# Performance work log

Hardware: AMD Instinct MI355X
Metric: run time of the kernel (lower is better)

Reference implementation:

```python
import jax, jax.numpy as jnp
import numpy as np
from jax import lax

H = 32   # hidden_size
L = 8    # num_layers
D_IN = 64    # lstm input_size / fc0 out
FEAT = 4096  # feature_size
T = 300      # frame_size
B = 64       # batch


def setup_inputs() -> dict:
    key = jax.random.key(0)
    ks = jax.random.split(key, 16)
    s = 0.05
    inp = {
        "x": jax.random.normal(ks[0], (B, T, FEAT), dtype=jnp.float32),
        # fc0: Linear(4096->64), ReLU, Dropout(eval), Linear(64->64)
        "W0": jax.random.normal(ks[1], (D_IN, FEAT), dtype=jnp.float32) * s,
        "b0": jax.random.normal(ks[2], (D_IN,), dtype=jnp.float32) * s,
        "W1": jax.random.normal(ks[3], (D_IN, D_IN), dtype=jnp.float32) * s,
        "b1": jax.random.normal(ks[4], (D_IN,), dtype=jnp.float32) * s,
        # LSTM params, PyTorch layout: W_ih [4H, in], W_hh [4H, H], biases [4H]
        "Wih0": jax.random.normal(ks[5], (4 * H, D_IN), dtype=jnp.float32) * s,
        "Wih": jax.random.normal(ks[6], (L - 1, 4 * H, H), dtype=jnp.float32) * s,
        "Whh": jax.random.normal(ks[7], (L, 4 * H, H), dtype=jnp.float32) * s,
        "bih": jax.random.normal(ks[8], (L, 4 * H), dtype=jnp.float32) * s,
        "bhh": jax.random.normal(ks[9], (L, 4 * H), dtype=jnp.float32) * s,
        # fc1: 32 -> 1 ; fc2: 300 -> 1
        "Wfc1": jax.random.normal(ks[10], (1, H), dtype=jnp.float32) * s,
        "bfc1": jax.random.normal(ks[11], (1,), dtype=jnp.float32) * s,
        "Wfc2": jax.random.normal(ks[12], (1, T), dtype=jnp.float32) * s,
        "bfc2": jax.random.normal(ks[13], (1,), dtype=jnp.float32) * s,
    }
    return inp


def _lstm_layer(x_seq, Wih_l, Whh_l, bih_l, bhh_l):
    # x_seq: [B, T, in] -> h_seq: [B, T, H]; PyTorch gate order i,f,g,o
    gx = jnp.einsum('bti,gi->btg', x_seq, Wih_l) + bih_l  # [B,T,4H]
    b = x_seq.shape[0]
    init = (jnp.zeros((b, H), x_seq.dtype), jnp.zeros((b, H), x_seq.dtype))

    def step(carry, gx_t):
        h, c = carry
        g = gx_t + h @ Whh_l.T + bhh_l
        i, f, gg, o = jnp.split(g, 4, axis=-1)
        c = jax.nn.sigmoid(f) * c + jax.nn.sigmoid(i) * jnp.tanh(gg)
        h = jax.nn.sigmoid(o) * jnp.tanh(c)
        return (h, c), h

    _, hs = lax.scan(step, init, jnp.swapaxes(gx, 0, 1))  # hs: [T,B,H]
    return jnp.swapaxes(hs, 0, 1)


def reference(x, W0, b0, W1, b1, Wih0, Wih, Whh, bih, bhh, Wfc1, bfc1, Wfc2, bfc2):
    # fc0 (dropout is identity in eval mode)
    h = jax.nn.relu(jnp.einsum('btf,of->bto', x, W0) + b0)
    h = jnp.einsum('bti,oi->bto', h, W1) + b1  # [B,T,64]
    # stacked LSTM, h0=c0=0
    for l in range(L):
        Wih_l = Wih0 if l == 0 else Wih[l - 1]
        h = _lstm_layer(h, Wih_l, Whh[l], bih[l], bhh[l])  # [B,T,32]
    # fc1 over hidden, squeeze, fc2 over time, squeeze
    y = jnp.einsum('bth,oh->bto', h, Wfc1)[..., 0] + bfc1[0]  # [B,T]
    y = y @ Wfc2.T + bfc2  # [B,1]
    return y[:, 0]
```

## Files before the change

### kernel.cpp

```cpp
#include <hip/hip_runtime.h>
#include <cstdint>

#define FEAT 4096
#define DIN  64
#define HS   32
#define NL   8
#define TT   300
#define BB   64
#define G4   128
#define MROWS (BB*TT)
#define KS    4
#define KSLICE (FEAT/KS)
#define BK    64
#define NCHUNK (KSLICE/BK)

typedef __bf16 bf16x8 __attribute__((ext_vector_type(8)));
typedef float  f32x4  __attribute__((ext_vector_type(4)));
typedef unsigned short u16x8 __attribute__((ext_vector_type(8)));

__device__ __forceinline__ float sigm(float x){ return __fdividef(1.f, 1.f + __expf(-x)); }
__device__ __forceinline__ float tanh_f(float x){ return __fdividef(2.f, 1.f + __expf(-2.f*x)) - 1.f; }

__device__ __forceinline__ unsigned short bf16_rne(float f){
    uint32_t u = __float_as_uint(f);
    return (unsigned short)((u + 0x7FFFu + ((u >> 16) & 1u)) >> 16);
}

__global__ __launch_bounds__(256) void w0split(const float* __restrict__ W0,
                                               unsigned short* __restrict__ wh,
                                               unsigned short* __restrict__ wl)
{
    const int i = (blockIdx.x * 256 + threadIdx.x) * 4;
    float4 v = *(const float4*)(W0 + i);
    float f[4] = {v.x, v.y, v.z, v.w};
    unsigned short hh[4], ll[4];
    #pragma unroll
    for (int j = 0; j < 4; ++j) {
        unsigned short h = bf16_rne(f[j]);
        float fh = __uint_as_float((uint32_t)h << 16);
        hh[j] = h;
        ll[j] = bf16_rne(f[j] - fh);
    }
    *(ushort4*)(wh + i) = make_ushort4(hh[0], hh[1], hh[2], hh[3]);
    *(ushort4*)(wl + i) = make_ushort4(ll[0], ll[1], ll[2], ll[3]);
}

__global__ __launch_bounds__(256, 2) void fc_gemm1(
    const float* __restrict__ x,
    const unsigned short* __restrict__ wh,
    const unsigned short* __restrict__ wl,
    float* __restrict__ part)
{
    __shared__ __align__(16) unsigned short xh[2][64][64];
    __shared__ __align__(16) unsigned short xl[2][64][64];
    __shared__ __align__(16) unsigned short wh_s[2][64][64];
    __shared__ __align__(16) unsigned short wl_s[2][64][64];

    const int t   = threadIdx.x;
    const int l   = t & 63;
    const int w   = t >> 6;
    const int rbb = (w >> 1) * 32;
    const int cbb = (w & 1) * 32;
    const int r0  = blockIdx.x * 64;
    const int kb0 = blockIdx.y * KSLICE;

    const int srow = t >> 3;
    const int sg   = t & 7;

    f32x4 acc[2][2];
    #pragma unroll
    for (int i = 0; i < 2; ++i)
        #pragma unroll
        for (int j = 0; j < 2; ++j)
            acc[i][j] = (f32x4){0.f, 0.f, 0.f, 0.f};

    float4 xr[2][2];
    uint4  w0h[2], w0l[2];

    auto LOAD = [&](int c) {
        const float* xb = x + (size_t)r0 * FEAT + kb0 + c * BK;
        xr[0][0] = *(const float4*)(xb + (size_t)srow * FEAT + sg * 8);
        xr[0][1] = *(const float4*)(xb + (size_t)srow * FEAT + sg * 8 + 4);
        xr[1][0] = *(const float4*)(xb + (size_t)(srow + 32) * FEAT + sg * 8);
        xr[1][1] = *(const float4*)(xb + (size_t)(srow + 32) * FEAT + sg * 8 + 4);
        const int wo = kb0 + c * BK + sg * 8;
        w0h[0] = *(const uint4*)(wh + (size_t)srow * FEAT + wo);
        w0h[1] = *(const uint4*)(wh + (size_t)(srow + 32) * FEAT + wo);
        w0l[0] = *(const uint4*)(wl + (size_t)srow * FEAT + wo);
        w0l[1] = *(const uint4*)(wl + (size_t)(srow + 32) * FEAT + wo);
    };

    auto STORE = [&](int c) {
        const int buf = c & 1;
        #pragma unroll
        for (int j = 0; j < 2; ++j) {
            const int row = srow + j * 32;
            const int gsw = (sg ^ (row & 7)) * 8;
            float f0[8] = {xr[j][0].x, xr[j][0].y, xr[j][0].z, xr[j][0].w,
                           xr[j][1].x, xr[j][1].y, xr[j][1].z, xr[j][1].w};
            u16x8 vh, vl;
            #pragma unroll
            for (int i = 0; i < 8; ++i) {
                uint32_t u  = __float_as_uint(f0[i]);
                uint32_t rh = (u + 0x7FFFu + ((u >> 16) & 1u)) >> 16;
                vh[i] = (unsigned short)rh;
                float fl = f0[i] - __uint_as_float(rh << 16);
                uint32_t u2 = __float_as_uint(fl);
                vl[i] = (unsigned short)((u2 + 0x7FFFu + ((u2 >> 16) & 1u)) >> 16);
            }
            *(u16x8*)&xh[buf][row][gsw] = vh;
            *(u16x8*)&xl[buf][row][gsw] = vl;
            *(uint4*)&wh_s[buf][row][gsw] = w0h[j];
            *(uint4*)&wl_s[buf][row][gsw] = w0l[j];
        }
    };

    auto COMPUTE = [&](int buf) {
        #pragma unroll
        for (int kstep = 0; kstep < 2; ++kstep) {
            const int gA = kstep * 4 + (l >> 4);
            bf16x8 Ah[2], Al[2], Bh[2], Bl[2];
            #pragma unroll
            for (int rf = 0; rf < 2; ++rf) {
                const int ra  = rbb + rf * 16 + (l & 15);
                const int off = (gA ^ (ra & 7)) * 8;
                Ah[rf] = __builtin_bit_cast(bf16x8, *(const u16x8*)&xh[buf][ra][off]);
                Al[rf] = __builtin_bit_cast(bf16x8, *(const u16x8*)&xl[buf][ra][off]);
            }
            #pragma unroll
            for (int cf = 0; cf < 2; ++cf) {
                const int cb  = cbb + cf * 16 + (l & 15);
                const int off = (gA ^ (cb & 7)) * 8;
                Bh[cf] = __builtin_bit_cast(bf16x8, *(const u16x8*)&wh_s[buf][cb][off]);
                Bl[cf] = __builtin_bit_cast(bf16x8, *(const u16x8*)&wl_s[buf][cb][off]);
            }
            #pragma unroll
            for (int rf = 0; rf < 2; ++rf)
                #pragma unroll
                for (int cf = 0; cf < 2; ++cf) {
                    acc[rf][cf] = __builtin_amdgcn_mfma_f32_16x16x32_bf16(Ah[rf], Bh[cf], acc[rf][cf], 0, 0, 0);
                    acc[rf][cf] = __builtin_amdgcn_mfma_f32_16x16x32_bf16(Al[rf], Bh[cf], acc[rf][cf], 0, 0, 0);
                    acc[rf][cf] = __builtin_amdgcn_mfma_f32_16x16x32_bf16(Ah[rf], Bl[cf], acc[rf][cf], 0, 0, 0);
                }
        }
    };

    LOAD(0);
    for (int c = 0; c < NCHUNK; ++c) {
        STORE(c);
        if (c + 1 < NCHUNK) LOAD(c + 1);
        asm volatile("s_waitcnt lgkmcnt(0)" ::: "memory");
        __builtin_amdgcn_s_barrier();
        COMPUTE(c & 1);
    }

    #pragma unroll
    for (int rf = 0; rf < 2; ++rf)
        #pragma unroll
        for (int cf = 0; cf < 2; ++cf)
            #pragma unroll
            for (int r = 0; r < 4; ++r) {
                const int row = r0 + rbb + rf * 16 + (l >> 4) * 4 + r;
                const int col = cbb + cf * 16 + (l & 15);
                part[((size_t)blockIdx.y * MROWS + row) * 64 + col] = acc[rf][cf][r];
            }
}

__global__ __launch_bounds__(256) void fc_tail(
    const float* __restrict__ part, const float* __restrict__ b0,
    const float* __restrict__ W1, const float* __restrict__ b1,
    const float* __restrict__ Wih0,
    const float* __restrict__ bih, const float* __restrict__ bhh,
    float* __restrict__ gx0)
{
    __shared__ __align__(16) float h1s[64][68];
    __shared__ __align__(16) float h2s[64][68];

    const int tid = threadIdx.x;
    const int tc  = tid & 15;
    const int tr  = tid >> 4;
    const int r0  = blockIdx.x * 64;

    {
        const int row = tid >> 2;
        const int c0  = (tid & 3) * 16;
        float4 s[4];
        #pragma unroll
        for (int i = 0; i < 4; ++i)
            s[i] = *(const float4*)(part + ((size_t)(r0 + row)) * 64 + c0 + 4 * i);
        #pragma unroll
        for (int ks = 1; ks < KS; ++ks)
            #pragma unroll
            for (int i = 0; i < 4; ++i) {
                float4 v = *(const float4*)(part + ((size_t)ks * MROWS + r0 + row) * 64 + c0 + 4 * i);
                s[i].x += v.x; s[i].y += v.y; s[i].z += v.z; s[i].w += v.w;
            }
        #pragma unroll
        for (int i = 0; i < 4; ++i) {
            float4 bv = *(const float4*)(b0 + c0 + 4 * i);
            float4 o;
            o.x = fmaxf(s[i].x + bv.x, 0.f);
            o.y = fmaxf(s[i].y + bv.y, 0.f);
            o.z = fmaxf(s[i].z + bv.z, 0.f);
            o.w = fmaxf(s[i].w + bv.w, 0.f);
            *(float4*)&h1s[row][c0 + 4 * i] = o;
        }
    }
    __syncthreads();

    float acc2[4][4] = {};
    #pragma unroll
    for (int k4 = 0; k4 < 16; ++k4) {
        const int k = k4 * 4;
        float4 a[4], wv[4];
        #pragma unroll
        for (int i = 0; i < 4; ++i) a[i] = *(const float4*)&h1s[tr * 4 + i][k];
        #pragma unroll
        for (int j = 0; j < 4; ++j) wv[j] = *(const float4*)(W1 + (size_t)(tc * 4 + j) * DIN + k);
        #pragma unroll
        for (int i = 0; i < 4; ++i)
            #pragma unroll
            for (int j = 0; j < 4; ++j)
                acc2[i][j] += a[i].x * wv[j].x + a[i].y * wv[j].y + a[i].z * wv[j].z + a[i].w * wv[j].w;
    }
    __syncthreads();
    #pragma unroll
    for (int i = 0; i < 4; ++i)
        #pragma unroll
        for (int j = 0; j < 4; ++j)
            h2s[tr * 4 + i][tc * 4 + j] = acc2[i][j] + b1[tc * 4 + j];
    __syncthreads();

    #pragma unroll
    for (int p = 0; p < 2; ++p) {
        float acc3[4][4] = {};
        #pragma unroll
        for (int k4 = 0; k4 < 16; ++k4) {
            const int k = k4 * 4;
            float4 a[4], wv[4];
            #pragma unroll
            for (int i = 0; i < 4; ++i) a[i] = *(const float4*)&h2s[tr * 4 + i][k];
            #pragma unroll
            for (int j = 0; j < 4; ++j) wv[j] = *(const float4*)(Wih0 + (size_t)(p * 64 + tc * 4 + j) * DIN + k);
            #pragma unroll
            for (int i = 0; i < 4; ++i)
                #pragma unroll
                for (int j = 0; j < 4; ++j)
                    acc3[i][j] += a[i].x * wv[j].x + a[i].y * wv[j].y + a[i].z * wv[j].z + a[i].w * wv[j].w;
        }
        const int g0 = p * 64 + tc * 4;
        #pragma unroll
        for (int i = 0; i < 4; ++i) {
            float4 ov;
            ov.x = acc3[i][0] + bih[g0 + 0] + bhh[g0 + 0];
            ov.y = acc3[i][1] + bih[g0 + 1] + bhh[g0 + 1];
            ov.z = acc3[i][2] + bih[g0 + 2] + bhh[g0 + 2];
            ov.w = acc3[i][3] + bih[g0 + 3] + bhh[g0 + 3];
            *(float4*)(gx0 + (size_t)(r0 + tr * 4 + i) * G4 + g0) = ov;
        }
    }
}

__global__ __launch_bounds__(512, 2) void lstm_all(
    const float* __restrict__ gx0,
    const float* __restrict__ Wih, const float* __restrict__ Whh,
    const float* __restrict__ bih, const float* __restrict__ bhh,
    const float* __restrict__ Wfc1, const float* __restrict__ bfc1,
    const float* __restrict__ Wfc2, const float* __restrict__ bfc2,
    float* __restrict__ out)
{
    const int b    = blockIdx.x;
    const int tid  = threadIdx.x;
    const int l    = tid >> 6;
    const int lane = tid & 63;
    const int q0   = lane;
    const int q1   = lane + 64;

    __shared__ __align__(16) float hbuf[NL][2][HS];
    __shared__ __align__(16) float gbuf[NL][G4];
    __shared__ __align__(16) float h7[TT][HS];
    __shared__ float red[NL];

    float whh0[HS], whh1[HS], wih0[HS], wih1[HS];
    {
        const float* whhl = Whh + (size_t)l * G4 * HS;
        const float* wihl = Wih + (size_t)(l > 0 ? l - 1 : 0) * G4 * HS;
        #pragma unroll
        for (int k4 = 0; k4 < 8; ++k4) {
            float4 v0 = *(const float4*)(whhl + q0 * HS + 4 * k4);
            float4 v1 = *(const float4*)(whhl + q1 * HS + 4 * k4);
            whh0[4*k4+0]=v0.x; whh0[4*k4+1]=v0.y; whh0[4*k4+2]=v0.z; whh0[4*k4+3]=v0.w;
            whh1[4*k4+0]=v1.x; whh1[4*k4+1]=v1.y; whh1[4*k4+2]=v1.z; whh1[4*k4+3]=v1.w;
            float4 u0 = *(const float4*)(wihl + q0 * HS + 4 * k4);
            float4 u1 = *(const float4*)(wihl + q1 * HS + 4 * k4);
            wih0[4*k4+0]=u0.x; wih0[4*k4+1]=u0.y; wih0[4*k4+2]=u0.z; wih0[4*k4+3]=u0.w;
            wih1[4*k4+0]=u1.x; wih1[4*k4+1]=u1.y; wih1[4*k4+2]=u1.z; wih1[4*k4+3]=u1.w;
        }
    }
    const float bias0 = (l > 0) ? (bih[l*G4 + q0] + bhh[l*G4 + q0]) : 0.f;
    const float bias1 = (l > 0) ? (bih[l*G4 + q1] + bhh[l*G4 + q1]) : 0.f;

    float c_state = 0.f;

    const float* gxb = gx0 + (size_t)b * TT * G4;
    float pf0 = 0.f, pf1 = 0.f;
    if (l == 0) { pf0 = gxb[q0]; pf1 = gxb[q1]; }

    for (int s = 0; s < TT + NL - 1; ++s) {
        const int t = s - l;
        if (0 <= t && t < TT) {
            float acc0, acc1;
            if (l == 0) {
                acc0 = pf0; acc1 = pf1;
                const int tn = t + 1;
                if (tn < TT) { pf0 = gxb[(size_t)tn * G4 + q0]; pf1 = gxb[(size_t)tn * G4 + q1]; }
            } else {
                acc0 = bias0; acc1 = bias1;
            }
            float a0a = 0.f, a0b = 0.f, a1a = 0.f, a1b = 0.f;
            if (t > 0) {
                const float4* hp = (const float4*)hbuf[l][(t - 1) & 1];
                #pragma unroll
                for (int k4 = 0; k4 < 8; ++k4) {
                    float4 v = hp[k4];
                    a0a = fmaf(whh0[4*k4+0], v.x, a0a); a0b = fmaf(whh0[4*k4+1], v.y, a0b);
                    a0a = fmaf(whh0[4*k4+2], v.z, a0a); a0b = fmaf(whh0[4*k4+3], v.w, a0b);
                    a1a = fmaf(whh1[4*k4+0], v.x, a1a); a1b = fmaf(whh1[4*k4+1], v.y, a1b);
                    a1a = fmaf(whh1[4*k4+2], v.z, a1a); a1b = fmaf(whh1[4*k4+3], v.w, a1b);
                }
            }
            if (l > 0) {
                const float4* hq = (const float4*)hbuf[l - 1][t & 1];
                #pragma unroll
                for (int k4 = 0; k4 < 8; ++k4) {
                    float4 v = hq[k4];
                    a0a = fmaf(wih0[4*k4+0], v.x, a0a); a0b = fmaf(wih0[4*k4+1], v.y, a0b);
                    a0a = fmaf(wih0[4*k4+2], v.z, a0a); a0b = fmaf(wih0[4*k4+3], v.w, a0b);
                    a1a = fmaf(wih1[4*k4+0], v.x, a1a); a1b = fmaf(wih1[4*k4+1], v.y, a1b);
                    a1a = fmaf(wih1[4*k4+2], v.z, a1a); a1b = fmaf(wih1[4*k4+3], v.w, a1b);
                }
            }
            acc0 += a0a + a0b;
            acc1 += a1a + a1b;
            gbuf[l][q0] = acc0;
            gbuf[l][q1] = acc1;
            asm volatile("s_waitcnt lgkmcnt(0)" ::: "memory");
            if (lane < HS) {
                const float ig = gbuf[l][lane];
                const float fg = gbuf[l][HS + lane];
                const float gg = gbuf[l][2*HS + lane];
                const float og = gbuf[l][3*HS + lane];
                c_state = sigm(fg) * c_state + sigm(ig) * tanh_f(gg);
                const float hv = sigm(og) * tanh_f(c_state);
                hbuf[l][t & 1][lane] = hv;
                if (l == NL - 1) h7[t][lane] = hv;
            }
        }
        __syncthreads();
    }

    float part = 0.f;
    for (int t = tid; t < TT; t += 512) {
        float st = 0.f;
        #pragma unroll
        for (int j = 0; j < HS; ++j) st = fmaf(h7[t][j], Wfc1[j], st);
        part += (st + bfc1[0]) * Wfc2[t];
    }
    #pragma unroll
    for (int off = 32; off >= 1; off >>= 1) part += __shfl_down(part, off, 64);
    if (lane == 0) red[l] = part;
    __syncthreads();
    if (tid == 0) {
        float tot = 0.f;
        #pragma unroll
        for (int w = 0; w < NL; ++w) tot += red[w];
        out[b] = tot + bfc2[0];
    }
}

extern "C" void kernel_launch(void* const* d_in, const int* in_sizes, int n_in,
                              void* d_out, int out_size, void* d_ws, size_t ws_size,
                              hipStream_t stream) {
    const float* x    = (const float*)d_in[0];
    const float* W0   = (const float*)d_in[1];
    const float* b0   = (const float*)d_in[2];
    const float* W1   = (const float*)d_in[3];
    const float* b1   = (const float*)d_in[4];
    const float* Wih0 = (const float*)d_in[5];
    const float* Wih  = (const float*)d_in[6];
    const float* Whh  = (const float*)d_in[7];
    const float* bih  = (const float*)d_in[8];
    const float* bhh  = (const float*)d_in[9];
    const float* Wfc1 = (const float*)d_in[10];
    const float* bfc1 = (const float*)d_in[11];
    const float* Wfc2 = (const float*)d_in[12];
    const float* bfc2 = (const float*)d_in[13];

    char* wsb = (char*)d_ws;
    float*          gx0 = (float*)wsb;
    unsigned short* wh  = (unsigned short*)(wsb + 9830400);
    unsigned short* wl  = (unsigned short*)(wsb + 9830400 + 524288);
    float*          prt = (float*)(wsb + 9830400 + 1048576);

    w0split <<<256, 256, 0, stream>>>(W0, wh, wl);
    fc_gemm1<<<dim3(MROWS / 64, KS), 256, 0, stream>>>(x, wh, wl, prt);
    fc_tail <<<MROWS / 64, 256, 0, stream>>>(prt, b0, W1, b1, Wih0, bih, bhh, gx0);
    lstm_all<<<BB, 512, 0, stream>>>(gx0, Wih, Whh, bih, bhh, Wfc1, bfc1, Wfc2, bfc2,
                                     (float*)d_out);
}
```

Baseline: 432.3 us.

## Split LSTM gate dot products across half-waves and reduce with shuffles

Each lane now computes all four gates for one hidden unit over half of the K dimension, and the two halves are combined with a cross-half shuffle. This removes the shared-memory gate buffer round trip and the lgkmcnt wait inside every recurrent step. The fc_tail output is interleaved per hidden unit so layer 0 fetches its four gate inputs with one float4 load. Weight loads go through pinned inline-asm loads and launch bounds drop to one block per CU, which could raise register pressure or change scheduling.

```diff
diff --git a/kernel.cpp b/kernel.cpp
--- a/kernel.cpp
+++ b/kernel.cpp
@@ -26,6 +26,20 @@
     return (unsigned short)((u + 0x7FFFu + ((u >> 16) & 1u)) >> 16);
 }
 
+__device__ __forceinline__ void ld4_pin(const float* p0, const float* p1,
+                                        const float* p2, const float* p3,
+                                        float4& a, float4& b, float4& c, float4& d) {
+    asm volatile(
+        "global_load_dwordx4 %0, %4, off\n\t"
+        "global_load_dwordx4 %1, %5, off\n\t"
+        "global_load_dwordx4 %2, %6, off\n\t"
+        "global_load_dwordx4 %3, %7, off\n\t"
+        "s_waitcnt vmcnt(0)"
+        : "=&v"(a), "=&v"(b), "=&v"(c), "=&v"(d)
+        : "v"(p0), "v"(p1), "v"(p2), "v"(p3)
+        : "memory");
+}
+
 __global__ __launch_bounds__(256) void w0split(const float* __restrict__ W0,
                                                unsigned short* __restrict__ wh,
                                                unsigned short* __restrict__ wl)
@@ -171,7 +185,7 @@
     const float* __restrict__ W1, const float* __restrict__ b1,
     const float* __restrict__ Wih0,
     const float* __restrict__ bih, const float* __restrict__ bhh,
-    float* __restrict__ gx0)
+    float* __restrict__ gxp)
 {
     __shared__ __align__(16) float h1s[64][68];
     __shared__ __align__(16) float h2s[64][68];
@@ -251,18 +265,20 @@
         const int g0 = p * 64 + tc * 4;
         #pragma unroll
         for (int i = 0; i < 4; ++i) {
-            float4 ov;
-            ov.x = acc3[i][0] + bih[g0 + 0] + bhh[g0 + 0];
-            ov.y = acc3[i][1] + bih[g0 + 1] + bhh[g0 + 1];
-            ov.z = acc3[i][2] + bih[g0 + 2] + bhh[g0 + 2];
-            ov.w = acc3[i][3] + bih[g0 + 3] + bhh[g0 + 3];
-            *(float4*)(gx0 + (size_t)(r0 + tr * 4 + i) * G4 + g0) = ov;
-        }
-    }
-}
-
-__global__ __launch_bounds__(512, 2) void lstm_all(
-    const float* __restrict__ gx0,
+            #pragma unroll
+            for (int jj = 0; jj < 4; ++jj) {
+                const int cc  = tc * 4 + jj;
+                const int m   = cc & 31;
+                const int gi  = p * 2 + (cc >> 5);
+                const float v = acc3[i][jj] + bih[g0 + jj] + bhh[g0 + jj];
+                gxp[(size_t)(r0 + tr * 4 + i) * G4 + m * 4 + gi] = v;
+            }
+        }
+    }
+}
+
+__global__ __launch_bounds__(512, 1) void lstm_all(
+    const float* __restrict__ gxp,
     const float* __restrict__ Wih, const float* __restrict__ Whh,
     const float* __restrict__ bih, const float* __restrict__ bhh,
     const float* __restrict__ Wfc1, const float* __restrict__ bfc1,
@@ -273,85 +289,109 @@
     const int tid  = threadIdx.x;
     const int l    = tid >> 6;
     const int lane = tid & 63;
-    const int q0   = lane;
-    const int q1   = lane + 64;
+    const int m    = lane & 31;
+    const int k0   = (lane >> 5) * 16;
 
     __shared__ __align__(16) float hbuf[NL][2][HS];
-    __shared__ __align__(16) float gbuf[NL][G4];
     __shared__ __align__(16) float h7[TT][HS];
     __shared__ float red[NL];
 
-    float whh0[HS], whh1[HS], wih0[HS], wih1[HS];
+    float4 wh4[4][4], wi4[4][4];
     {
-        const float* whhl = Whh + (size_t)l * G4 * HS;
-        const float* wihl = Wih + (size_t)(l > 0 ? l - 1 : 0) * G4 * HS;
-        #pragma unroll
-        for (int k4 = 0; k4 < 8; ++k4) {
-            float4 v0 = *(const float4*)(whhl + q0 * HS + 4 * k4);
-            float4 v1 = *(const float4*)(whhl + q1 * HS + 4 * k4);
-            whh0[4*k4+0]=v0.x; whh0[4*k4+1]=v0.y; whh0[4*k4+2]=v0.z; whh0[4*k4+3]=v0.w;
-            whh1[4*k4+0]=v1.x; whh1[4*k4+1]=v1.y; whh1[4*k4+2]=v1.z; whh1[4*k4+3]=v1.w;
-            float4 u0 = *(const float4*)(wihl + q0 * HS + 4 * k4);
-            float4 u1 = *(const float4*)(wihl + q1 * HS + 4 * k4);
-            wih0[4*k4+0]=u0.x; wih0[4*k4+1]=u0.y; wih0[4*k4+2]=u0.z; wih0[4*k4+3]=u0.w;
-            wih1[4*k4+0]=u1.x; wih1[4*k4+1]=u1.y; wih1[4*k4+2]=u1.z; wih1[4*k4+3]=u1.w;
-        }
-    }
-    const float bias0 = (l > 0) ? (bih[l*G4 + q0] + bhh[l*G4 + q0]) : 0.f;
-    const float bias1 = (l > 0) ? (bih[l*G4 + q1] + bhh[l*G4 + q1]) : 0.f;
+        const float* wb = Whh + (size_t)l * G4 * HS;
+        #pragma unroll
+        for (int j = 0; j < 4; ++j) {
+            const float* rp = wb + (size_t)(j * 32 + m) * HS + k0;
+            ld4_pin(rp, rp + 4, rp + 8, rp + 12,
+                    wh4[j][0], wh4[j][1], wh4[j][2], wh4[j][3]);
+        }
+    }
+    if (l > 0) {
+        const float* wb = Wih + (size_t)(l - 1) * G4 * HS;
+        #pragma unroll
+        for (int j = 0; j < 4; ++j) {
+            const float* rp = wb + (size_t)(j * 32 + m) * HS + k0;
+            ld4_pin(rp, rp + 4, rp + 8, rp + 12,
+                    wi4[j][0], wi4[j][1], wi4[j][2], wi4[j][3]);
+        }
+    } else {
+        #pragma unroll
+        for (int j = 0; j < 4; ++j)
+            #pragma unroll
+            for (int q = 0; q < 4; ++q)
+                wi4[j][q] = make_float4(0.f, 0.f, 0.f, 0.f);
+    }
+
+    float bias[4] = {0.f, 0.f, 0.f, 0.f};
+    if (l > 0) {
+        #pragma unroll
+        for (int j = 0; j < 4; ++j)
+            bias[j] = bih[l * G4 + j * 32 + m] + bhh[l * G4 + j * 32 + m];
+    }
 
     float c_state = 0.f;
 
-    const float* gxb = gx0 + (size_t)b * TT * G4;
-    float pf0 = 0.f, pf1 = 0.f;
-    if (l == 0) { pf0 = gxb[q0]; pf1 = gxb[q1]; }
+    const float* gxb = gxp + (size_t)b * TT * G4;
+    float4 pf = make_float4(0.f, 0.f, 0.f, 0.f);
+    if (l == 0) pf = *(const float4*)(gxb + m * 4);
 
     for (int s = 0; s < TT + NL - 1; ++s) {
         const int t = s - l;
         if (0 <= t && t < TT) {
-            float acc0, acc1;
+            float4 gin;
             if (l == 0) {
-                acc0 = pf0; acc1 = pf1;
+                gin = pf;
                 const int tn = t + 1;
-                if (tn < TT) { pf0 = gxb[(size_t)tn * G4 + q0]; pf1 = gxb[(size_t)tn * G4 + q1]; }
-            } else {
-                acc0 = bias0; acc1 = bias1;
-            }
-            float a0a = 0.f, a0b = 0.f, a1a = 0.f, a1b = 0.f;
+                if (tn < TT) pf = *(const float4*)(gxb + (size_t)tn * G4 + m * 4);
+            }
+
+            float r0_ = 0.f, r1_ = 0.f, r2_ = 0.f, r3_ = 0.f;
             if (t > 0) {
-                const float4* hp = (const float4*)hbuf[l][(t - 1) & 1];
-                #pragma unroll
-                for (int k4 = 0; k4 < 8; ++k4) {
-                    float4 v = hp[k4];
-                    a0a = fmaf(whh0[4*k4+0], v.x, a0a); a0b = fmaf(whh0[4*k4+1], v.y, a0b);
-                    a0a = fmaf(whh0[4*k4+2], v.z, a0a); a0b = fmaf(whh0[4*k4+3], v.w, a0b);
-                    a1a = fmaf(whh1[4*k4+0], v.x, a1a); a1b = fmaf(whh1[4*k4+1], v.y, a1b);
-                    a1a = fmaf(whh1[4*k4+2], v.z, a1a); a1b = fmaf(whh1[4*k4+3], v.w, a1b);
+                const float* hp = hbuf[l][(t - 1) & 1];
+                float4 hv[4];
+                #pragma unroll
+                for (int q = 0; q < 4; ++q) hv[q] = *(const float4*)(hp + k0 + 4 * q);
+                #pragma unroll
+                for (int q = 0; q < 4; ++q) {
+                    r0_ = fmaf(wh4[0][q].x, hv[q].x, r0_); r0_ = fmaf(wh4[0][q].y, hv[q].y, r0_);
+                    r0_ = fmaf(wh4[0][q].z, hv[q].z, r0_); r0_ = fmaf(wh4[0][q].w, hv[q].w, r0_);
+                    r1_ = fmaf(wh4[1][q].x, hv[q].x, r1_); r1_ = fmaf(wh4[1][q].y, hv[q].y, r1_);
+                    r1_ = fmaf(wh4[1][q].z, hv[q].z, r1_); r1_ = fmaf(wh4[1][q].w, hv[q].w, r1_);
+                    r2_ = fmaf(wh4[2][q].x, hv[q].x, r2_); r2_ = fmaf(wh4[2][q].y, hv[q].y, r2_);
+                    r2_ = fmaf(wh4[2][q].z, hv[q].z, r2_); r2_ = fmaf(wh4[2][q].w, hv[q].w, r2_);
+                    r3_ = fmaf(wh4[3][q].x, hv[q].x, r3_); r3_ = fmaf(wh4[3][q].y, hv[q].y, r3_);
+                    r3_ = fmaf(wh4[3][q].z, hv[q].z, r3_); r3_ = fmaf(wh4[3][q].w, hv[q].w, r3_);
                 }
             }
             if (l > 0) {
-                const float4* hq = (const float4*)hbuf[l - 1][t & 1];
-                #pragma unroll
-                for (int k4 = 0; k4 < 8; ++k4) {
-                    float4 v = hq[k4];
-                    a0a = fmaf(wih0[4*k4+0], v.x, a0a); a0b = fmaf(wih0[4*k4+1], v.y, a0b);
-                    a0a = fmaf(wih0[4*k4+2], v.z, a0a); a0b = fmaf(wih0[4*k4+3], v.w, a0b);
-                    a1a = fmaf(wih1[4*k4+0], v.x, a1a); a1b = fmaf(wih1[4*k4+1], v.y, a1b);
-                    a1a = fmaf(wih1[4*k4+2], v.z, a1a); a1b = fmaf(wih1[4*k4+3], v.w, a1b);
+                const float* hq = hbuf[l - 1][t & 1];
+                float4 hv[4];
+                #pragma unroll
+                for (int q = 0; q < 4; ++q) hv[q] = *(const float4*)(hq + k0 + 4 * q);
+                #pragma unroll
+                for (int q = 0; q < 4; ++q) {
+                    r0_ = fmaf(wi4[0][q].x, hv[q].x, r0_); r0_ = fmaf(wi4[0][q].y, hv[q].y, r0_);
+                    r0_ = fmaf(wi4[0][q].z, hv[q].z, r0_); r0_ = fmaf(wi4[0][q].w, hv[q].w, r0_);
+                    r1_ = fmaf(wi4[1][q].x, hv[q].x, r1_); r1_ = fmaf(wi4[1][q].y, hv[q].y, r1_);
+                    r1_ = fmaf(wi4[1][q].z, hv[q].z, r1_); r1_ = fmaf(wi4[1][q].w, hv[q].w, r1_);
+                    r2_ = fmaf(wi4[2][q].x, hv[q].x, r2_); r2_ = fmaf(wi4[2][q].y, hv[q].y, r2_);
+                    r2_ = fmaf(wi4[2][q].z, hv[q].z, r2_); r2_ = fmaf(wi4[2][q].w, hv[q].w, r2_);
+                    r3_ = fmaf(wi4[3][q].x, hv[q].x, r3_); r3_ = fmaf(wi4[3][q].y, hv[q].y, r3_);
+                    r3_ = fmaf(wi4[3][q].z, hv[q].z, r3_); r3_ = fmaf(wi4[3][q].w, hv[q].w, r3_);
                 }
             }
-            acc0 += a0a + a0b;
-            acc1 += a1a + a1b;
-            gbuf[l][q0] = acc0;
-            gbuf[l][q1] = acc1;
-            asm volatile("s_waitcnt lgkmcnt(0)" ::: "memory");
+
+            float gi = r0_ + __shfl_xor(r0_, 32, 64);
+            float gf = r1_ + __shfl_xor(r1_, 32, 64);
+            float gg = r2_ + __shfl_xor(r2_, 32, 64);
+            float go = r3_ + __shfl_xor(r3_, 32, 64);
+            if (l == 0) { gi += gin.x; gf += gin.y; gg += gin.z; go += gin.w; }
+            else        { gi += bias[0]; gf += bias[1]; gg += bias[2]; go += bias[3]; }
+
+            c_state = sigm(gf) * c_state + sigm(gi) * tanh_f(gg);
+            const float hv = sigm(go) * tanh_f(c_state);
+
             if (lane < HS) {
-                const float ig = gbuf[l][lane];
-                const float fg = gbuf[l][HS + lane];
-                const float gg = gbuf[l][2*HS + lane];
-                const float og = gbuf[l][3*HS + lane];
-                c_state = sigm(fg) * c_state + sigm(ig) * tanh_f(gg);
-                const float hv = sigm(og) * tanh_f(c_state);
                 hbuf[l][t & 1][lane] = hv;
                 if (l == NL - 1) h7[t][lane] = hv;
             }
@@ -397,14 +437,14 @@
     const float* bfc2 = (const float*)d_in[13];
 
     char* wsb = (char*)d_ws;
-    float*          gx0 = (float*)wsb;
+    float*          gxp = (float*)wsb;
     unsigned short* wh  = (unsigned short*)(wsb + 9830400);
     unsigned short* wl  = (unsigned short*)(wsb + 9830400 + 524288);
     float*          prt = (float*)(wsb + 9830400 + 1048576);
 
     w0split <<<256, 256, 0, stream>>>(W0, wh, wl);
     fc_gemm1<<<dim3(MROWS / 64, KS), 256, 0, stream>>>(x, wh, wl, prt);
-    fc_tail <<<MROWS / 64, 256, 0, stream>>>(prt, b0, W1, b1, Wih0, bih, bhh, gx0);
-    lstm_all<<<BB, 512, 0, stream>>>(gx0, Wih, Whh, bih, bhh, Wfc1, bfc1, Wfc2, bfc2,
+    fc_tail <<<MROWS / 64, 256, 0, stream>>>(prt, b0, W1, b1, Wih0, bih, bhh, gxp);
+    lstm_all<<<BB, 512, 0, stream>>>(gxp, Wih, Whh, bih, bhh, Wfc1, bfc1, Wfc2, bfc2,
                                      (float*)d_out);
 }
```

Result: slower. 443.9 us (+2.7%).
